# Optimization experiments

Hardware: AMD Instinct MI355X
Metric: run time of the kernel (lower is better)

## Reference

```python
import jax, jax.numpy as jnp
import numpy as np

POOL = 7; SR = 2; SCALE = 1.0 / 16
NUM_CLASSES = 21
NMS_THR = 0.5; MIN_SIZE = 1.0; TOPK = 100; SCORE_THR = 0.05
BBOX_CLIP = float(np.log(1000.0 / 16))


def roi_align(feat, rois):
    # feat: [C,H,W]; rois: [P,4] xyxy in image coords. torchvision aligned=True, sampling_ratio=2.
    C, H, W = feat.shape
    S = POOL * SR
    x0r = rois[:, 0] * SCALE - 0.5
    y0r = rois[:, 1] * SCALE - 0.5
    bw = (rois[:, 2] - rois[:, 0]) * SCALE / POOL
    bh = (rois[:, 3] - rois[:, 1]) * SCALE / POOL
    t = (jnp.arange(S, dtype=feat.dtype) + 0.5) / SR  # sample offsets in bin units
    ys = y0r[:, None] + bh[:, None] * t  # [P,S]
    xs = x0r[:, None] + bw[:, None] * t  # [P,S]
    vy = (ys >= -1.0) & (ys <= H)
    vx = (xs >= -1.0) & (xs <= W)
    y = jnp.clip(ys, 0.0, H - 1)
    x = jnp.clip(xs, 0.0, W - 1)
    yl = jnp.floor(y).astype(jnp.int32); xl = jnp.floor(x).astype(jnp.int32)
    yh = jnp.minimum(yl + 1, H - 1);     xh = jnp.minimum(xl + 1, W - 1)
    ly = y - yl; lx = x - xl
    hy = 1.0 - ly; hx = 1.0 - lx

    def g(Yi, Xi):  # -> [C,P,S,S]
        return feat[:, Yi[:, :, None], Xi[:, None, :]]

    val = (g(yl, xl) * (hy[:, :, None] * hx[:, None, :])
         + g(yl, xh) * (hy[:, :, None] * lx[:, None, :])
         + g(yh, xl) * (ly[:, :, None] * hx[:, None, :])
         + g(yh, xh) * (ly[:, :, None] * lx[:, None, :]))
    val = val * (vy[:, :, None] & vx[:, None, :])[None].astype(feat.dtype)
    P = rois.shape[0]
    val = val.reshape(C, P, POOL, SR, POOL, SR).mean(axis=(3, 5))  # avg over 2x2 samples/bin
    return val.transpose(1, 0, 2, 3)  # [P,C,POOL,POOL]


def decode(pred, proposals):
    # pred: [N,K,4] (dx,dy,dw,dh); proposals: [N,4]
    w = proposals[:, 2] - proposals[:, 0]
    h = proposals[:, 3] - proposals[:, 1]
    cx = proposals[:, 0] + 0.5 * w
    cy = proposals[:, 1] + 0.5 * h
    dx, dy = pred[..., 0], pred[..., 1]
    dw = jnp.minimum(pred[..., 2], BBOX_CLIP)
    dh = jnp.minimum(pred[..., 3], BBOX_CLIP)
    pcx = dx * w[:, None] + cx[:, None]
    pcy = dy * h[:, None] + cy[:, None]
    pw = jnp.exp(dw) * w[:, None]
    ph = jnp.exp(dh) * h[:, None]
    return jnp.stack([pcx - 0.5 * pw, pcy - 0.5 * ph, pcx + 0.5 * pw, pcy + 0.5 * ph], axis=-1)


def box_iou(b):
    x1, y1, x2, y2 = b[:, 0], b[:, 1], b[:, 2], b[:, 3]
    area = (x2 - x1) * (y2 - y1)
    iw = jnp.maximum(jnp.minimum(x2[:, None], x2[None, :]) - jnp.maximum(x1[:, None], x1[None, :]), 0.0)
    ih = jnp.maximum(jnp.minimum(y2[:, None], y2[None, :]) - jnp.maximum(y1[:, None], y1[None, :]), 0.0)
    inter = iw * ih
    return inter / (area[:, None] + area[None, :] - inter)


def filter_predictions(boxes, labels, scores):
    # score threshold + min-size + per-class greedy NMS + topK, static shapes (padded to TOPK)
    N = scores.shape[0]
    ws = boxes[:, 2] - boxes[:, 0]
    hs = boxes[:, 3] - boxes[:, 1]
    valid = (scores > SCORE_THR) & (ws >= MIN_SIZE) & (hs >= MIN_SIZE)
    skey = jnp.where(valid, scores, -jnp.inf)
    order = jnp.argsort(-skey)
    b = boxes[order]; s = skey[order]; l = labels[order]; v = valid[order]
    # batched_nms via per-class coordinate offset
    off = jax.lax.stop_gradient(jnp.max(boxes) + 1.0)
    ob = jax.lax.stop_gradient(b) + (l.astype(b.dtype) * off)[:, None]
    iou = box_iou(ob)  # [N,N]
    idx = jnp.arange(N)

    def body(keep, i):
        sup = (iou[i] > NMS_THR) & keep[i] & (idx > i)
        return keep & ~sup, None

    keep, _ = jax.lax.scan(body, v, idx)
    rank = jnp.cumsum(keep) - 1
    final = keep & (rank < TOPK)
    pick = jnp.argsort(jnp.where(final, idx, N))[:TOPK]  # kept indices in score order, padded
    ok = final[pick]
    out_boxes = jnp.where(ok[:, None], b[pick], 0.0)
    out_scores = jnp.where(ok, s[pick], 0.0)
    out_labels = jnp.where(ok, l[pick], -1)
    return out_boxes, out_labels, out_scores


def roi_head_forward(image, feat, proposals, fc6_w, fc6_b, fc7_w, fc7_b, cls_w, cls_b, reg_w, reg_b):
    H_img, W_img = image.shape[-2], image.shape[-1]
    pooled = roi_align(feat[0], proposals)  # [P,C,7,7]
    x = pooled.reshape(pooled.shape[0], -1)
    x = jax.nn.relu(x @ fc6_w.T + fc6_b)
    x = jax.nn.relu(x @ fc7_w.T + fc7_b)
    cls_scores = x @ cls_w.T + cls_b                       # [P,K]
    box_pred = (x @ reg_w.T + reg_b).reshape(-1, NUM_CLASSES, 4)
    boxes = decode(box_pred, proposals)                    # [P,K,4]
    scores = jax.nn.softmax(cls_scores, axis=-1)
    boxes = jnp.stack([boxes[..., 0].clip(0, W_img), boxes[..., 1].clip(0, H_img),
                       boxes[..., 2].clip(0, W_img), boxes[..., 3].clip(0, H_img)], axis=-1)
    labels = jnp.broadcast_to(jnp.arange(NUM_CLASSES), scores.shape)
    boxes = boxes[:, 1:].reshape(-1, 4)
    scores = scores[:, 1:].reshape(-1)
    labels = (labels[:, 1:] - 1).reshape(-1)
    return filter_predictions(boxes, labels, scores)


def setup_inputs() -> dict:
    key = jax.random.key(0)
    ks = jax.random.split(key, 12)
    H_img, W_img = 800, 1072
    P, C = 300, 512
    image = jnp.zeros((1, 3, H_img, W_img), jnp.float32)
    feat = jax.random.normal(ks[0], (1, C, H_img // 16, W_img // 16), jnp.float32)
    cx = jax.random.uniform(ks[1], (P,)) * W_img
    cy = jax.random.uniform(ks[2], (P,)) * H_img
    bw = 20.0 + jax.random.uniform(ks[3], (P,)) * 300.0
    bh = 20.0 + jax.random.uniform(ks[4], (P,)) * 300.0
    proposals = jnp.stack([jnp.clip(cx - bw / 2, 0, W_img), jnp.clip(cy - bh / 2, 0, H_img),
                           jnp.clip(cx + bw / 2, 0, W_img), jnp.clip(cy + bh / 2, 0, H_img)], axis=1)
    fin = C * POOL * POOL  # 25088
    D = 1024
    fc6_w = jax.random.normal(ks[5], (D, fin), jnp.float32) / np.sqrt(fin)
    fc6_b = jnp.zeros((D,), jnp.float32)
    fc7_w = jax.random.normal(ks[6], (D, D), jnp.float32) / np.sqrt(D)
    fc7_b = jnp.zeros((D,), jnp.float32)
    cls_w = jax.random.normal(ks[7], (NUM_CLASSES, D), jnp.float32) / np.sqrt(D)
    cls_b = jnp.zeros((NUM_CLASSES,), jnp.float32)
    reg_w = jax.random.normal(ks[8], (NUM_CLASSES * 4, D), jnp.float32) * 0.001
    reg_b = jnp.zeros((NUM_CLASSES * 4,), jnp.float32)
    return {"image": image, "feat": feat, "proposals": proposals,
            "fc6_w": fc6_w, "fc6_b": fc6_b, "fc7_w": fc7_w, "fc7_b": fc7_b,
            "cls_w": cls_w, "cls_b": cls_b, "reg_w": reg_w, "reg_b": reg_b}


def reference(image, feat, proposals, fc6_w, fc6_b, fc7_w, fc7_b, cls_w, cls_b, reg_w, reg_b):
    return roi_head_forward(image, feat, proposals, fc6_w, fc6_b, fc7_w, fc7_b, cls_w, cls_b, reg_w, reg_b)
```

## Files before the change

### kernel.cpp

```cpp
#include <hip/hip_runtime.h>
#include <hip/hip_bf16.h>
#include <math.h>

#define P_N   300
#define C_N   512
#define H_F   50
#define W_F   67
#define HW_F  3350
#define D_N   1024
#define FIN   25088
#define NCLS  21
#define NCAND 6000
#define W_IMG 1072.0f
#define H_IMG 800.0f
#define BBOX_CLIP_F 4.135166556742356f
#define KS6   28
#define STEPS6_PER_Z 28
#define KS7   16
#define STEPS7_PER_Z 2
#define KSH   16
#define STEPSH_PER_Z 2
#define NHEAD 128
#define NW    96
#define A_SCALE 16.0f
#define B_SCALE 256.0f
#define O_SCALE (1.0f / 4096.0f)
#define TBLK  1680

typedef __attribute__((ext_vector_type(8)))  _Float16 half8;
typedef __attribute__((ext_vector_type(16))) float    f32x16;

__device__ __forceinline__ void splitA(float f, _Float16& h, _Float16& l) {
  float fs = f * A_SCALE;
  h = (_Float16)fs;
  l = (_Float16)(fs - (float)h);
}

__device__ __forceinline__ int swz(int slot, int ks) {
  return slot ^ ((slot >> 5) & 1) ^ (((slot >> 3) & 1) << 1) ^ ((ks & 1) << 2);
}

__device__ __forceinline__ int blob_half_idx(int row, int j8) {
  const int ksW = j8 >> 1, kc8 = j8 & 1;
  const int mf = row >> 5;
  return (mf * 2 + ksW) * 512 + swz((kc8 << 5) | (row & 31), ksW) * 8;
}

__global__ __launch_bounds__(256) void prep_transpose(const float* __restrict__ feat,
                                                      float* __restrict__ ft,
                                                      const float* __restrict__ cls_w,
                                                      const float* __restrict__ cls_b,
                                                      const float* __restrict__ reg_w,
                                                      const float* __restrict__ reg_b,
                                                      float* __restrict__ Wpad,
                                                      float* __restrict__ bpad,
                                                      int* __restrict__ vcount) {
  __shared__ float tile[32][33];
  const int bid = blockIdx.x;
  const int tid = threadIdx.x;
  if (bid < TBLK) {
    const int bx = bid % 105, byy = bid / 105;
    const int s0 = bx * 32, c0 = byy * 32;
    const int tx = tid & 31, ty = tid >> 5;
    for (int r = ty; r < 32; r += 8) {
      int c = c0 + r, s = s0 + tx;
      tile[r][tx] = (s < HW_F) ? feat[(size_t)c * HW_F + s] : 0.0f;
    }
    __syncthreads();
    for (int r = ty; r < 32; r += 8) {
      int s = s0 + r, c = c0 + tx;
      if (s < HW_F) ft[(size_t)s * C_N + c] = tile[tx][r];
    }
  } else {
    const int row = bid - TBLK;
    if (row == 0 && tid == 0) *vcount = 0;
    const float* src = (row < NCLS) ? (cls_w + (size_t)row * D_N)
                     : (row < 105)  ? (reg_w + (size_t)(row - NCLS) * D_N) : nullptr;
    float4 v = make_float4(0.f, 0.f, 0.f, 0.f);
    if (src) v = reinterpret_cast<const float4*>(src)[tid];
    reinterpret_cast<float4*>(Wpad + (size_t)row * D_N)[tid] = v;
    if (tid == 0)
      bpad[row] = (row < NCLS) ? cls_b[row] : (row < 105) ? reg_b[row - NCLS] : 0.0f;
  }
}

__global__ __launch_bounds__(256, 3) void roi_align_k(const float* __restrict__ ft,
                                                      const float* __restrict__ rois,
                                                      _Float16* __restrict__ Xhi,
                                                      _Float16* __restrict__ Xlo) {
  __shared__ _Float16 hbuf[12544] __attribute__((aligned(16)));
  __shared__ _Float16 lbuf[12544] __attribute__((aligned(16)));
  __shared__ float g_ly[14], g_hy[14], g_lx[14], g_hx[14];
  __shared__ int   g_yoL[14], g_yoH[14], g_xoL[14], g_xoH[14];

  const int p   = blockIdx.x;
  const int ch  = blockIdx.y;
  const int tid = threadIdx.x;

  if (tid < 14) {
    const float rx0 = rois[p*4+0], ry0 = rois[p*4+1], rx1 = rois[p*4+2], ry1 = rois[p*4+3];
    const float x0r = rx0 * 0.0625f - 0.5f;
    const float y0r = ry0 * 0.0625f - 0.5f;
    const float bw  = (rx1 - rx0) * 0.0625f * (1.0f / 7.0f);
    const float bh  = (ry1 - ry0) * 0.0625f * (1.0f / 7.0f);
    const float t   = ((float)tid + 0.5f) * 0.5f;

    const float ys = y0r + bh * t;
    const bool vy = (ys >= -1.0f) && (ys <= (float)H_F);
    float y = fminf(fmaxf(ys, 0.0f), (float)(H_F - 1));
    int yi = (int)floorf(y);
    const int yh = min(yi + 1, H_F - 1);
    float ly = y - (float)yi, hy = 1.0f - (y - (float)yi);
    if (!vy) { ly = 0.0f; hy = 0.0f; }
    g_ly[tid] = ly; g_hy[tid] = hy;
    g_yoL[tid] = yi * (W_F * C_N); g_yoH[tid] = yh * (W_F * C_N);

    const float xs = x0r + bw * t;
    const bool vx = (xs >= -1.0f) && (xs <= (float)W_F);
    float x = fminf(fmaxf(xs, 0.0f), (float)(W_F - 1));
    int xi = (int)floorf(x);
    const int xh = min(xi + 1, W_F - 1);
    float lx = x - (float)xi, hx = 1.0f - (x - (float)xi);
    if (!vx) { lx = 0.0f; hx = 0.0f; }
    g_lx[tid] = lx; g_hx[tid] = hx;
    g_xoL[tid] = xi * C_N; g_xoH[tid] = xh * C_N;
  }
  __syncthreads();

  const float* ftc = ft + ch * 256 + tid;
#pragma unroll 4
  for (int cell = 0; cell < 49; ++cell) {
    const int py = cell / 7;
    const int px = cell - py * 7;
    float acc = 0.0f;
#pragma unroll
    for (int sy = 0; sy < 2; ++sy) {
      const int iy = 2 * py + sy;
      const float ly = g_ly[iy], hy = g_hy[iy];
      const int yoL = g_yoL[iy], yoH = g_yoH[iy];
#pragma unroll
      for (int sx = 0; sx < 2; ++sx) {
        const int ix = 2 * px + sx;
        const float lx = g_lx[ix], hx = g_hx[ix];
        const int xoL = g_xoL[ix], xoH = g_xoH[ix];
        acc += (hy*hx)*ftc[yoL+xoL] + (hy*lx)*ftc[yoL+xoH]
             + (ly*hx)*ftc[yoH+xoL] + (ly*lx)*ftc[yoH+xoH];
      }
    }
    _Float16 h, l;
    splitA(acc * 0.25f, h, l);
    hbuf[tid * 49 + cell] = h;
    lbuf[tid * 49 + cell] = l;
  }
  __syncthreads();

  const size_t base = (size_t)p * FIN + (size_t)ch * 12544;
  const uint4* hs = (const uint4*)hbuf;
  const uint4* ls = (const uint4*)lbuf;
  uint4* dh = (uint4*)(Xhi + base);
  uint4* dl = (uint4*)(Xlo + base);
  for (int k = tid; k < 1568; k += 256) { dh[k] = hs[k]; dl[k] = ls[k]; }
}

__global__ __launch_bounds__(256) void reshuffle_x(const _Float16* __restrict__ Shi,
                                                   const _Float16* __restrict__ Slo,
                                                   char* __restrict__ blob,
                                                   int M2, int K) {
  __shared__ _Float16 buf[8192] __attribute__((aligned(16)));
  const int tile = blockIdx.x, step = blockIdx.y;
  const int tid = threadIdx.x;
  const int steps = K >> 5;
#pragma unroll
  for (int i = 0; i < 4; ++i) {
    const int g = tid + i * 256;
    const int half = g >> 9;
    const int row = (g >> 2) & 127;
    const int j8 = g & 3;
    const int gm = tile * 128 + row;
    uint4 v = make_uint4(0, 0, 0, 0);
    if (gm < M2) {
      const _Float16* src = (half ? Slo : Shi) + (size_t)gm * K + (step << 5) + (j8 << 3);
      v = *reinterpret_cast<const uint4*>(src);
    }
    *reinterpret_cast<uint4*>(buf + half * 4096 + blob_half_idx(row, j8)) = v;
  }
  __syncthreads();
  uint4* dst = (uint4*)(blob + (((size_t)tile * steps + step) << 14));
  const uint4* s = (const uint4*)buf;
#pragma unroll
  for (int i = 0; i < 4; ++i) dst[tid + i * 256] = s[tid + i * 256];
}

__global__ __launch_bounds__(256) void gemm_f16_3p(
    const char* __restrict__ Ablob, const float* __restrict__ Wt, float* __restrict__ Pt,
    int M, int K, int steps_per_z, int ldc)
{
  __shared__ _Float16 lds[32768] __attribute__((aligned(16)));
  const int tid  = threadIdx.x;
  const int lane = tid & 63, wave = tid >> 6;
  const int wm = wave >> 1, wn = wave & 1;

  const int GX = gridDim.x, GY = gridDim.y;
  const int T  = GX * GY * gridDim.z;
  int flat = blockIdx.x + GX * (blockIdx.y + GY * blockIdx.z);
  if ((T & 7) == 0) flat = (flat & 7) * (T >> 3) + (flat >> 3);
  const int bx = flat % GX;
  const int by = (flat / GX) % GY;
  const int bz = flat / (GX * GY);

  const int m0 = bx * 128, n0 = by * 128;
  const int steps_total = K >> 5;
  const int s0 = bz * steps_per_z;
  const int s1 = min(s0 + steps_per_z, steps_total);

  f32x16 acc[2][2];
#pragma unroll
  for (int a = 0; a < 2; ++a)
#pragma unroll
    for (int b = 0; b < 2; ++b)
#pragma unroll
      for (int r = 0; r < 16; ++r) acc[a][b][r] = 0.f;

  const int srow = tid >> 2;
  const int j8   = tid & 3;
  const int ksW  = j8 >> 1, kc8 = j8 & 1;
  const int wslot = swz((kc8 << 5) | (srow & 31), ksW);
  const int nf0 = srow >> 5;
  const int nf1 = (srow + 64) >> 5;

  for (int s = s0; s < s1; s += 2) {
    const char* Ab = Ablob + (((size_t)bx * steps_total + s) << 14);
#pragma unroll
    for (int c2 = 0; c2 < 8; ++c2) {
      const int off = ((wave << 3) + c2) << 10;
      __builtin_amdgcn_global_load_lds(
          (const __attribute__((address_space(1))) uint32_t*)(Ab + off + (lane << 4)),
          (__attribute__((address_space(3))) uint32_t*)((char*)lds + off),
          16, 0, 0);
    }
#pragma unroll
    for (int sub = 0; sub < 2; ++sub) {
      const int kb = (s + sub) << 5;
#pragma unroll
      for (int half = 0; half < 2; ++half) {
        const int n = srow + half * 64;
        const float* wp = Wt + (size_t)(n0 + n) * K + kb + j8 * 8;
        const float4 f0 = *reinterpret_cast<const float4*>(wp);
        const float4 f1 = *reinterpret_cast<const float4*>(wp + 4);
        float fv[8] = {f0.x, f0.y, f0.z, f0.w, f1.x, f1.y, f1.z, f1.w};
        union { _Float16 h[8]; uint4 v; } uh, ul;
#pragma unroll
        for (int e = 0; e < 8; ++e) {
          float fs = fv[e] * B_SCALE;
          uh.h[e] = (_Float16)fs;
          ul.h[e] = (_Float16)(fs - (float)uh.h[e]);
        }
        const int nf = half ? nf1 : nf0;
        const int base = 16384 + sub * 8192 + (nf * 2 + ksW) * 512 + wslot * 8;
        *reinterpret_cast<uint4*>(&lds[base])        = uh.v;
        *reinterpret_cast<uint4*>(&lds[4096 + base]) = ul.v;
      }
    }
    __syncthreads();
#pragma unroll
    for (int sub = 0; sub < 2; ++sub) {
      _Float16* ldsA = lds + sub * 8192;
      _Float16* ldsB = lds + 16384 + sub * 8192;
#pragma unroll
      for (int ks = 0; ks < 2; ++ks) {
        const int rslot = swz(lane, ks) * 8;
        half8 ah[2], al[2], bh[2], bl[2];
#pragma unroll
        for (int mi = 0; mi < 2; ++mi) {
          const int mf = wm * 2 + mi;
          ah[mi] = *reinterpret_cast<const half8*>(&ldsA[(mf * 2 + ks) * 512 + rslot]);
          al[mi] = *reinterpret_cast<const half8*>(&ldsA[4096 + (mf * 2 + ks) * 512 + rslot]);
        }
#pragma unroll
        for (int ni = 0; ni < 2; ++ni) {
          const int nf = wn * 2 + ni;
          bh[ni] = *reinterpret_cast<const half8*>(&ldsB[(nf * 2 + ks) * 512 + rslot]);
          bl[ni] = *reinterpret_cast<const half8*>(&ldsB[4096 + (nf * 2 + ks) * 512 + rslot]);
        }
#pragma unroll
        for (int mi = 0; mi < 2; ++mi)
#pragma unroll
          for (int ni = 0; ni < 2; ++ni) {
            acc[mi][ni] = __builtin_amdgcn_mfma_f32_32x32x16_f16(ah[mi], bh[ni], acc[mi][ni], 0, 0, 0);
            acc[mi][ni] = __builtin_amdgcn_mfma_f32_32x32x16_f16(ah[mi], bl[ni], acc[mi][ni], 0, 0, 0);
            acc[mi][ni] = __builtin_amdgcn_mfma_f32_32x32x16_f16(al[mi], bh[ni], acc[mi][ni], 0, 0, 0);
          }
      }
    }
    __syncthreads();
  }
  const int col = lane & 31, rhi = lane >> 5;
  float* outp = Pt + (size_t)bz * ((size_t)M * ldc);
#pragma unroll
  for (int mi = 0; mi < 2; ++mi)
#pragma unroll
    for (int ni = 0; ni < 2; ++ni) {
      const int n = n0 + (wn * 2 + ni) * 32 + col;
      if (n >= ldc) continue;
#pragma unroll
      for (int r = 0; r < 16; ++r) {
        const int m = m0 + (wm * 2 + mi) * 32 + ((r & 3) + 8 * (r >> 2) + 4 * rhi);
        if (m < M) outp[(size_t)m * ldc + n] = acc[mi][ni][r] * O_SCALE;
      }
    }
}

__global__ __launch_bounds__(256) void reduce_frag(const float* __restrict__ Pt,
                                                   const float* __restrict__ bias,
                                                   char* __restrict__ blob,
                                                   int KS, int stepsB) {
  const int g = blockIdx.x * 256 + threadIdx.x;
  if (g >= P_N * 128) return;
  const int m = g >> 7;
  const int gg = g & 127;
  const int n0 = gg << 3;
  float s[8];
#pragma unroll
  for (int e = 0; e < 8; ++e) s[e] = bias[n0 + e];
  for (int k2 = 0; k2 < KS; ++k2) {
    const float* pp = Pt + ((size_t)k2 * P_N + m) * D_N + n0;
    const float4 a = *reinterpret_cast<const float4*>(pp);
    const float4 b = *reinterpret_cast<const float4*>(pp + 4);
    s[0]+=a.x; s[1]+=a.y; s[2]+=a.z; s[3]+=a.w;
    s[4]+=b.x; s[5]+=b.y; s[6]+=b.z; s[7]+=b.w;
  }
  union { _Float16 h[8]; uint4 v; } uh, ul;
#pragma unroll
  for (int e = 0; e < 8; ++e) {
    float r = fmaxf(s[e], 0.0f);
    _Float16 h, l; splitA(r, h, l);
    uh.h[e] = h; ul.h[e] = l;
  }
  const int tile = m >> 7, row = m & 127;
  const int step = gg >> 2, j8 = gg & 3;
  _Float16* dst = (_Float16*)(blob + (((size_t)tile * stepsB + step) << 14));
  const int hidx = blob_half_idx(row, j8);
  *reinterpret_cast<uint4*>(dst + hidx) = uh.v;
  *reinterpret_cast<uint4*>(dst + 4096 + hidx) = ul.v;
}

__global__ __launch_bounds__(64) void decode_kernel(const float* __restrict__ Pt,
                                                    const float* __restrict__ bpad,
                                                    const float* __restrict__ props,
                                                    float* __restrict__ cboxes,
                                                    unsigned long long* __restrict__ ckeys,
                                                    int* __restrict__ vcount) {
  const int p = blockIdx.x;
  const int lane = threadIdx.x;
  __shared__ float lg[NHEAD];

  for (int o = lane; o < NHEAD; o += 64) {
    float s = 0.0f;
    for (int k = 0; k < KSH; ++k)
      s += Pt[((size_t)k * P_N + p) * NHEAD + o];
    lg[o] = s + bpad[o];
  }
  __syncthreads();

  float s = (lane < NCLS) ? lg[lane] : -__builtin_inff();
  float mx = s;
#pragma unroll
  for (int off = 32; off > 0; off >>= 1) mx = fmaxf(mx, __shfl_xor(mx, off));
  float e = (lane < NCLS) ? expf(s - mx) : 0.0f;
  float sum = e;
#pragma unroll
  for (int off = 32; off > 0; off >>= 1) sum += __shfl_xor(sum, off);
  const float sm = e / sum;

  if (lane >= 1 && lane < NCLS) {
    const int c = lane;
    const float x0 = props[p*4+0], y0 = props[p*4+1], x1 = props[p*4+2], y1 = props[p*4+3];
    const float w = x1 - x0, hh = y1 - y0;
    const float cx = x0 + 0.5f * w, cy = y0 + 0.5f * hh;
    const float dx = lg[NCLS + c*4 + 0];
    const float dy = lg[NCLS + c*4 + 1];
    const float dw = fminf(lg[NCLS + c*4 + 2], BBOX_CLIP_F);
    const float dh = fminf(lg[NCLS + c*4 + 3], BBOX_CLIP_F);
    const float pcx = dx * w + cx, pcy = dy * hh + cy;
    const float pw = expf(dw) * w, ph = expf(dh) * hh;
    float bx0 = pcx - 0.5f * pw, by0 = pcy - 0.5f * ph;
    float bx1 = pcx + 0.5f * pw, by1 = pcy + 0.5f * ph;
    bx0 = fminf(fmaxf(bx0, 0.0f), W_IMG);
    by0 = fminf(fmaxf(by0, 0.0f), H_IMG);
    bx1 = fminf(fmaxf(bx1, 0.0f), W_IMG);
    by1 = fminf(fmaxf(by1, 0.0f), H_IMG);
    const int idx = p * 20 + (c - 1);
    cboxes[idx*4+0] = bx0; cboxes[idx*4+1] = by0;
    cboxes[idx*4+2] = bx1; cboxes[idx*4+3] = by1;
    const bool valid = (sm > 0.05f) && ((bx1 - bx0) >= 1.0f) && ((by1 - by0) >= 1.0f);
    if (valid) {
      int pos = atomicAdd(vcount, 1);
      unsigned u = __float_as_uint(sm);
      ckeys[pos] = ((unsigned long long)(~u) << 32) | (unsigned)idx;
    }
  }
}

__global__ __launch_bounds__(1024) void sort_gather(const unsigned long long* __restrict__ ckeys,
                                                    const int* __restrict__ vcount,
                                                    const float* __restrict__ cboxes,
                                                    float4* __restrict__ sbox,
                                                    float* __restrict__ sscore,
                                                    int* __restrict__ slab) {
  __shared__ unsigned long long keys[8192];
  const int tid = threadIdx.x;
  const int V = *vcount;
  int Npad = 64; while (Npad < V) Npad <<= 1;
  for (int i = tid; i < Npad; i += 1024)
    keys[i] = (i < V) ? ckeys[i] : ~0ULL;
  __syncthreads();
  for (int kk = 2; kk <= Npad; kk <<= 1) {
    for (int j = kk >> 1; j > 0; j >>= 1) {
      for (int i = tid; i < Npad; i += 1024) {
        int ij = i ^ j;
        if (ij > i) {
          unsigned long long a = keys[i], b = keys[ij];
          bool up = ((i & kk) == 0);
          if ((a > b) == up) { keys[i] = b; keys[ij] = a; }
        }
      }
      __syncthreads();
    }
  }
  for (int i = tid; i < V; i += 1024) {
    unsigned long long key = keys[i];
    int idx = (int)(key & 0xffffffffu);
    sbox[i]   = *reinterpret_cast<const float4*>(&cboxes[(size_t)idx * 4]);
    sscore[i] = __uint_as_float(~(unsigned)(key >> 32));
    slab[i]   = idx % 20;
  }
}

__global__ __launch_bounds__(256) void iou_matrix(const float4* __restrict__ sbox,
                                                  const int* __restrict__ slab,
                                                  const int* __restrict__ vcount,
                                                  unsigned long long* __restrict__ mask) {
  const int V = *vcount;
  const int i = blockIdx.x * 4 + (threadIdx.x >> 6);
  const int lane = threadIdx.x & 63;
  if (i >= V) return;
  const float4 bi = sbox[i];
  const int li = slab[i];
  const float ai = (bi.z - bi.x) * (bi.w - bi.y);
  const int nw = (V + 63) >> 6;
  for (int w = 0; w < nw; ++w) {
    const int j = (w << 6) + lane;
    bool sup = false;
    if (j > i && j < V && slab[j] == li) {
      const float4 bj = sbox[j];
      const float iw = fminf(bi.z, bj.z) - fmaxf(bi.x, bj.x);
      const float ih = fminf(bi.w, bj.w) - fmaxf(bi.y, bj.y);
      const float inter = fmaxf(iw, 0.0f) * fmaxf(ih, 0.0f);
      const float aj = (bj.z - bj.x) * (bj.w - bj.y);
      sup = inter / (ai + aj - inter) > 0.5f;
    }
    const unsigned long long m = __ballot(sup);
    if (lane == 0) mask[(size_t)i * NW + w] = m;
  }
}

__device__ __forceinline__ unsigned long long bcast_live(unsigned long long live0,
                                                         unsigned long long live1, int w) {
  union { unsigned long long u; uint2 v; } t;
  t.u = (w < 64) ? live0 : live1;
  const int src = w & 63;
  const unsigned lo = __shfl(t.v.x, src);
  const unsigned hi = __shfl(t.v.y, src);
  return ((unsigned long long)hi << 32) | lo;
}

__global__ __launch_bounds__(64) void nms_scan(const float4* __restrict__ sbox,
                                               const float* __restrict__ sscore,
                                               const int* __restrict__ slab,
                                               const int* __restrict__ vcount,
                                               const unsigned long long* __restrict__ mask,
                                               float* __restrict__ out) {
  const int lane = threadIdx.x;
  const int V = min(*vcount, NCAND);
  const int nw = (V + 63) >> 6;
  unsigned long long live0 = ~0ULL, live1 = ~0ULL;
  int nk = 0;
  for (int w = 0; w < nw && nk < 100; ++w) {
    const int nb = V - (w << 6);
    const unsigned long long vmask = (nb >= 64) ? ~0ULL : ((1ULL << nb) - 1ULL);
    unsigned long long wv = bcast_live(live0, live1, w) & vmask;
    while (wv && nk < 100) {
      const int b = __ffsll((long long)wv) - 1;
      const int i = (w << 6) + b;
      if (lane == 0) {
        const float4 bb = sbox[i];
        out[nk*4+0] = bb.x; out[nk*4+1] = bb.y; out[nk*4+2] = bb.z; out[nk*4+3] = bb.w;
        out[400 + nk] = (float)slab[i];
        out[500 + nk] = sscore[i];
      }
      const unsigned long long* mrow = mask + (size_t)i * NW;
      if (lane < nw) live0 &= ~mrow[lane];
      if (64 + lane < nw) live1 &= ~mrow[64 + lane];
      nk++;
      wv = bcast_live(live0, live1, w) & vmask;
      wv &= (b == 63) ? 0ULL : ~((2ULL << b) - 1ULL);
    }
  }
  for (int r = nk + lane; r < 100; r += 64) {
    out[r*4+0] = 0.0f; out[r*4+1] = 0.0f; out[r*4+2] = 0.0f; out[r*4+3] = 0.0f;
    out[400 + r] = -1.0f;
    out[500 + r] = 0.0f;
  }
}

extern "C" void kernel_launch(void* const* d_in, const int* in_sizes, int n_in,
                              void* d_out, int out_size, void* d_ws, size_t ws_size,
                              hipStream_t stream) {
  const float* feat   = (const float*)d_in[1];
  const float* props  = (const float*)d_in[2];
  const float* fc6_w  = (const float*)d_in[3];
  const float* fc6_b  = (const float*)d_in[4];
  const float* fc7_w  = (const float*)d_in[5];
  const float* fc7_b  = (const float*)d_in[6];
  const float* cls_w  = (const float*)d_in[7];
  const float* cls_b  = (const float*)d_in[8];
  const float* reg_w  = (const float*)d_in[9];
  const float* reg_b  = (const float*)d_in[10];

  char* ws = (char*)d_ws;
  const size_t XSZ = (size_t)P_N * FIN * 2;
  const size_t R1  = (size_t)KS6 * P_N * D_N * 4;
  _Float16* Xhi = (_Float16*)ws;
  _Float16* Xlo = (_Float16*)(ws + XSZ);
  float*    Pt  = (float*)ws;
  char* reg2 = ws + R1;
  float* ft   = (float*)reg2;
  char*  Xb   = reg2;
  const size_t XBSZ = (size_t)3 * 784 * 16384;
  size_t off = R1 + XBSZ;
  auto alloc = [&](size_t bytes) -> void* {
    void* p = ws + off;
    off += (bytes + 255) & ~(size_t)255;
    return p;
  };
  char*  h6b   = (char*)alloc((size_t)3 * 32 * 16384);
  char*  h7b   = (char*)alloc((size_t)3 * 32 * 16384);
  float* Wpad  = (float*)alloc((size_t)NHEAD * D_N * 4);
  float* bpad  = (float*)alloc((size_t)NHEAD * 4);
  float* cboxes= (float*)alloc((size_t)NCAND * 4 * 4);
  unsigned long long* ckeys = (unsigned long long*)alloc((size_t)NCAND * 8);
  float4* sbox = (float4*)alloc((size_t)NCAND * 16);
  float* sscore= (float*)alloc((size_t)NCAND * 4);
  int*   slab  = (int*)alloc((size_t)NCAND * 4);
  unsigned long long* supmask = (unsigned long long*)alloc((size_t)NCAND * NW * 8);
  int*   vcount= (int*)alloc(256);
  (void)ws_size; (void)in_sizes; (void)n_in; (void)out_size;

  prep_transpose<<<TBLK + NHEAD, 256, 0, stream>>>(feat, ft, cls_w, cls_b, reg_w, reg_b,
                                                   Wpad, bpad, vcount);
  roi_align_k<<<dim3(P_N, 2), 256, 0, stream>>>(ft, props, Xhi, Xlo);
  reshuffle_x<<<dim3(3, 784), 256, 0, stream>>>(Xhi, Xlo, Xb, P_N, FIN);
  gemm_f16_3p<<<dim3(3, 8, KS6), 256, 0, stream>>>(Xb, fc6_w, Pt, P_N, FIN, STEPS6_PER_Z, D_N);
  reduce_frag<<<150, 256, 0, stream>>>(Pt, fc6_b, h6b, KS6, 32);
  gemm_f16_3p<<<dim3(3, 8, KS7), 256, 0, stream>>>(h6b, fc7_w, Pt, P_N, D_N, STEPS7_PER_Z, D_N);
  reduce_frag<<<150, 256, 0, stream>>>(Pt, fc7_b, h7b, KS7, 32);
  gemm_f16_3p<<<dim3(3, 1, KSH), 256, 0, stream>>>(h7b, Wpad, Pt, P_N, D_N, STEPSH_PER_Z, NHEAD);
  decode_kernel<<<P_N, 64, 0, stream>>>(Pt, bpad, props, cboxes, ckeys, vcount);
  sort_gather<<<1, 1024, 0, stream>>>(ckeys, vcount, cboxes, sbox, sscore, slab);
  iou_matrix<<<(NCAND + 3) / 4, 256, 0, stream>>>(sbox, slab, vcount, supmask);
  nms_scan<<<1, 64, 0, stream>>>(sbox, sscore, slab, vcount, supmask, (float*)d_out);
}
```

Before: 355.6 us.

## Double-buffer GEMM LDS stages to overlap loads with MFMA compute

Restructures the split-precision f16 GEMM main loop from processing two k-steps per iteration, with a load/sync/compute/sync pattern, into a one-step double-buffered pipeline. The next step's A blob and converted W tiles are staged into the alternate LDS buffer while the current buffer is consumed, and compute is bracketed with s_setprio. This drops one barrier per step and aims to hide global-load latency. Launch bounds now request 2 blocks per CU, which may limit registers available for the 64 accumulator values per thread.

```diff
diff --git a/kernel.cpp b/kernel.cpp
--- a/kernel.cpp
+++ b/kernel.cpp
@@ -191,7 +191,7 @@
   for (int i = 0; i < 4; ++i) dst[tid + i * 256] = s[tid + i * 256];
 }
 
-__global__ __launch_bounds__(256) void gemm_f16_3p(
+__global__ __launch_bounds__(256, 2) void gemm_f16_3p(
     const char* __restrict__ Ablob, const float* __restrict__ Wt, float* __restrict__ Pt,
     int M, int K, int steps_per_z, int ldc)
 {
@@ -225,75 +225,82 @@
   const int j8   = tid & 3;
   const int ksW  = j8 >> 1, kc8 = j8 & 1;
   const int wslot = swz((kc8 << 5) | (srow & 31), ksW);
-  const int nf0 = srow >> 5;
-  const int nf1 = (srow + 64) >> 5;
-
-  for (int s = s0; s < s1; s += 2) {
-    const char* Ab = Ablob + (((size_t)bx * steps_total + s) << 14);
-#pragma unroll
-    for (int c2 = 0; c2 < 8; ++c2) {
-      const int off = ((wave << 3) + c2) << 10;
+
+  auto stage = [&](int buf, int step) {
+    const char* Ab = Ablob + (((size_t)bx * steps_total + step) << 14);
+    char* ldsb = (char*)lds + (buf << 15);
+#pragma unroll
+    for (int c2 = 0; c2 < 4; ++c2) {
+      const int off = ((wave << 2) + c2) << 10;
       __builtin_amdgcn_global_load_lds(
           (const __attribute__((address_space(1))) uint32_t*)(Ab + off + (lane << 4)),
-          (__attribute__((address_space(3))) uint32_t*)((char*)lds + off),
+          (__attribute__((address_space(3))) uint32_t*)(ldsb + off),
           16, 0, 0);
     }
-#pragma unroll
-    for (int sub = 0; sub < 2; ++sub) {
-      const int kb = (s + sub) << 5;
-#pragma unroll
-      for (int half = 0; half < 2; ++half) {
-        const int n = srow + half * 64;
-        const float* wp = Wt + (size_t)(n0 + n) * K + kb + j8 * 8;
-        const float4 f0 = *reinterpret_cast<const float4*>(wp);
-        const float4 f1 = *reinterpret_cast<const float4*>(wp + 4);
-        float fv[8] = {f0.x, f0.y, f0.z, f0.w, f1.x, f1.y, f1.z, f1.w};
-        union { _Float16 h[8]; uint4 v; } uh, ul;
-#pragma unroll
-        for (int e = 0; e < 8; ++e) {
-          float fs = fv[e] * B_SCALE;
-          uh.h[e] = (_Float16)fs;
-          ul.h[e] = (_Float16)(fs - (float)uh.h[e]);
+    _Float16* ldsh = (_Float16*)ldsb;
+    const int kb = step << 5;
+#pragma unroll
+    for (int half = 0; half < 2; ++half) {
+      const int n = srow + half * 64;
+      const float* wp = Wt + (size_t)(n0 + n) * K + kb + j8 * 8;
+      const float4 f0 = *reinterpret_cast<const float4*>(wp);
+      const float4 f1 = *reinterpret_cast<const float4*>(wp + 4);
+      float fv[8] = {f0.x, f0.y, f0.z, f0.w, f1.x, f1.y, f1.z, f1.w};
+      union { _Float16 h[8]; uint4 v; } uh, ul;
+#pragma unroll
+      for (int e = 0; e < 8; ++e) {
+        float fs = fv[e] * B_SCALE;
+        uh.h[e] = (_Float16)fs;
+        ul.h[e] = (_Float16)(fs - (float)uh.h[e]);
+      }
+      const int nf = n >> 5;
+      const int base = 8192 + (nf * 2 + ksW) * 512 + wslot * 8;
+      *reinterpret_cast<uint4*>(&ldsh[base])        = uh.v;
+      *reinterpret_cast<uint4*>(&ldsh[4096 + base]) = ul.v;
+    }
+  };
+
+  auto compute = [&](int buf) {
+    _Float16* ldsh = (_Float16*)((char*)lds + (buf << 15));
+#pragma unroll
+    for (int ks = 0; ks < 2; ++ks) {
+      const int rslot = swz(lane, ks) * 8;
+      half8 ah[2], al[2], bh[2], bl[2];
+#pragma unroll
+      for (int mi = 0; mi < 2; ++mi) {
+        const int mf = wm * 2 + mi;
+        ah[mi] = *reinterpret_cast<const half8*>(&ldsh[(mf * 2 + ks) * 512 + rslot]);
+        al[mi] = *reinterpret_cast<const half8*>(&ldsh[4096 + (mf * 2 + ks) * 512 + rslot]);
+      }
+#pragma unroll
+      for (int ni = 0; ni < 2; ++ni) {
+        const int nf = wn * 2 + ni;
+        bh[ni] = *reinterpret_cast<const half8*>(&ldsh[8192  + (nf * 2 + ks) * 512 + rslot]);
+        bl[ni] = *reinterpret_cast<const half8*>(&ldsh[12288 + (nf * 2 + ks) * 512 + rslot]);
+      }
+#pragma unroll
+      for (int mi = 0; mi < 2; ++mi)
+#pragma unroll
+        for (int ni = 0; ni < 2; ++ni) {
+          acc[mi][ni] = __builtin_amdgcn_mfma_f32_32x32x16_f16(ah[mi], bh[ni], acc[mi][ni], 0, 0, 0);
+          acc[mi][ni] = __builtin_amdgcn_mfma_f32_32x32x16_f16(ah[mi], bl[ni], acc[mi][ni], 0, 0, 0);
+          acc[mi][ni] = __builtin_amdgcn_mfma_f32_32x32x16_f16(al[mi], bh[ni], acc[mi][ni], 0, 0, 0);
         }
-        const int nf = half ? nf1 : nf0;
-        const int base = 16384 + sub * 8192 + (nf * 2 + ksW) * 512 + wslot * 8;
-        *reinterpret_cast<uint4*>(&lds[base])        = uh.v;
-        *reinterpret_cast<uint4*>(&lds[4096 + base]) = ul.v;
-      }
-    }
+    }
+  };
+
+  if (s0 < s1) stage(0, s0);
+  __syncthreads();
+  int cur = 0;
+  for (int s = s0; s < s1; ++s) {
+    if (s + 1 < s1) stage(cur ^ 1, s + 1);
+    __builtin_amdgcn_s_setprio(1);
+    compute(cur);
+    __builtin_amdgcn_s_setprio(0);
     __syncthreads();
-#pragma unroll
-    for (int sub = 0; sub < 2; ++sub) {
-      _Float16* ldsA = lds + sub * 8192;
-      _Float16* ldsB = lds + 16384 + sub * 8192;
-#pragma unroll
-      for (int ks = 0; ks < 2; ++ks) {
-        const int rslot = swz(lane, ks) * 8;
-        half8 ah[2], al[2], bh[2], bl[2];
-#pragma unroll
-        for (int mi = 0; mi < 2; ++mi) {
-          const int mf = wm * 2 + mi;
-          ah[mi] = *reinterpret_cast<const half8*>(&ldsA[(mf * 2 + ks) * 512 + rslot]);
-          al[mi] = *reinterpret_cast<const half8*>(&ldsA[4096 + (mf * 2 + ks) * 512 + rslot]);
-        }
-#pragma unroll
-        for (int ni = 0; ni < 2; ++ni) {
-          const int nf = wn * 2 + ni;
-          bh[ni] = *reinterpret_cast<const half8*>(&ldsB[(nf * 2 + ks) * 512 + rslot]);
-          bl[ni] = *reinterpret_cast<const half8*>(&ldsB[4096 + (nf * 2 + ks) * 512 + rslot]);
-        }
-#pragma unroll
-        for (int mi = 0; mi < 2; ++mi)
-#pragma unroll
-          for (int ni = 0; ni < 2; ++ni) {
-            acc[mi][ni] = __builtin_amdgcn_mfma_f32_32x32x16_f16(ah[mi], bh[ni], acc[mi][ni], 0, 0, 0);
-            acc[mi][ni] = __builtin_amdgcn_mfma_f32_32x32x16_f16(ah[mi], bl[ni], acc[mi][ni], 0, 0, 0);
-            acc[mi][ni] = __builtin_amdgcn_mfma_f32_32x32x16_f16(al[mi], bh[ni], acc[mi][ni], 0, 0, 0);
-          }
-      }
-    }
-    __syncthreads();
-  }
+    cur ^= 1;
+  }
+
   const int col = lane & 31, rhi = lane >> 5;
   float* outp = Pt + (size_t)bz * ((size_t)M * ldc);
 #pragma unroll
```

Result: no change. 360.5 us (+1.4%).
